# Kernel optimization log

Measured on AMD Instinct MI355X. Metric: run time of the kernel, lower is better.

## Reference

```python
import jax, jax.numpy as jnp
import numpy as np

VAR_SCALE = 0.1


def setup_inputs() -> dict:
    key = jax.random.key(0)
    k_x, k_tc, k_task, k_in, k_out = jax.random.split(key, 5)
    B, T, IN, OUT, R = 1024, 8, 4096, 4096, 64
    x = jax.random.normal(k_x, (B, T, IN), dtype=jnp.float32)
    tensor_core = jax.random.normal(k_tc, (R, R, R), dtype=jnp.float32) * VAR_SCALE
    task_core = jax.random.normal(k_task, (T, R), dtype=jnp.float32) * VAR_SCALE
    in_core = jax.random.normal(k_in, (IN, R), dtype=jnp.float32) * VAR_SCALE
    out_core = jax.random.normal(k_out, (OUT, R), dtype=jnp.float32) * VAR_SCALE
    return {"x": x, "tensor_core": tensor_core, "task_core": task_core,
            "in_core": in_core, "out_core": out_core}


def reference(x, tensor_core, task_core, in_core, out_core):
    # Tucker weight reconstruction, faithful to the torch einsum chain.
    # W1: [T, R, R] = task_core @ tensor_core (contract first core mode)
    W = jnp.einsum('tj,jkl->tkl', task_core, tensor_core)
    # W2: [T, IN, R] = contract in_core with middle mode
    W = jnp.einsum('ij,tjk->tik', in_core, W)
    # W3: [T, IN, OUT] = contract out_core with last mode
    W = jnp.einsum('oj,tij->tio', out_core, W)
    # Batched per-task matmul: x [B, T, IN] -> y [B, T, OUT]
    y = jnp.einsum('bti,tio->bto', x, W)
    return y
```

## Files before the change

kernel.cpp:

```cpp
#include <hip/hip_runtime.h>
#include <hip/hip_bf16.h>


typedef __bf16 bf16;
typedef __bf16 bf16x8 __attribute__((ext_vector_type(8)));
typedef __bf16 bf16x4 __attribute__((ext_vector_type(4)));
typedef float  f32x4  __attribute__((ext_vector_type(4)));

__device__ __forceinline__ bf16x8 load_frag_bf16(const bf16* p) {
    return *reinterpret_cast<const bf16x8*>(p);
}

__device__ __forceinline__ bf16x8 load_frag_f32(const float* p) {
    f32x4 a = *reinterpret_cast<const f32x4*>(p);
    f32x4 b = *reinterpret_cast<const f32x4*>(p + 4);
    bf16x8 r;
    r[0] = (bf16)a[0]; r[1] = (bf16)a[1]; r[2] = (bf16)a[2]; r[3] = (bf16)a[3];
    r[4] = (bf16)b[0]; r[5] = (bf16)b[1]; r[6] = (bf16)b[2]; r[7] = (bf16)b[3];
    return r;
}

__device__ __forceinline__ f32x4 mfma16(bf16x8 a, bf16x8 b, f32x4 c) {
    return __builtin_amdgcn_mfma_f32_16x16x32_bf16(a, b, c, 0, 0, 0);
}

__global__ __launch_bounds__(256) void k_setup(
    const float* __restrict__ task,
    const float* __restrict__ tensor,
    const float* __restrict__ in_core,
    bf16* __restrict__ w1,
    bf16* __restrict__ icT)
{
    int bid = blockIdx.x;
    if (bid < 128) {
        int t    = bid >> 4;
        int idx  = (bid & 15) * 256 + threadIdx.x;
        int j    = idx >> 6;
        int k    = idx & 63;
        float acc = 0.f;
        #pragma unroll 8
        for (int m = 0; m < 64; ++m)
            acc += task[t * 64 + m] * tensor[(m * 64 + j) * 64 + k];
        w1[(t * 64 + j) * 64 + k] = (bf16)acc;
    } else {
        int idx = (bid - 128) * 256 + threadIdx.x;
        int i0  = (idx & 511) * 8;
        int j   = idx >> 9;
        bf16x8 v;
        #pragma unroll
        for (int s = 0; s < 8; ++s)
            v[s] = (bf16)in_core[(size_t)(i0 + s) * 64 + j];
        *reinterpret_cast<bf16x8*>(icT + (size_t)j * 4096 + i0) = v;
    }
}

__global__ __launch_bounds__(256) void k2_mt(
    const float* __restrict__ out_core,
    const bf16* __restrict__ w1,
    bf16* __restrict__ mt)
{
    int t    = blockIdx.x >> 6;
    int ot   = blockIdx.x & 63;
    int wave = threadIdx.x >> 6;
    int lane = threadIdx.x & 63;
    int m    = lane & 15;
    int q    = lane >> 4;
    int o0   = ot * 64 + wave * 16;

    f32x4 acc[4] = {};
    #pragma unroll
    for (int kc = 0; kc < 64; kc += 32) {
        bf16x8 a = load_frag_f32(out_core + (size_t)(o0 + m) * 64 + kc + q * 8);
        #pragma unroll
        for (int nt = 0; nt < 4; ++nt) {
            bf16x8 b = load_frag_bf16(w1 + (size_t)(t * 64 + nt * 16 + m) * 64 + kc + q * 8);
            acc[nt] = mfma16(a, b, acc[nt]);
        }
    }
    #pragma unroll
    for (int nt = 0; nt < 4; ++nt) {
        #pragma unroll
        for (int r = 0; r < 4; ++r) {
            int o = o0 + q * 4 + r;
            mt[(size_t)(t * 4096 + o) * 64 + nt * 16 + m] = (bf16)acc[nt][r];
        }
    }
}

__global__ __launch_bounds__(256) void k_fused(
    const float* __restrict__ x,
    const bf16* __restrict__ icT,
    const bf16* __restrict__ mt,
    float* __restrict__ y)
{
    __shared__ bf16  xs[16 * 256];
    __shared__ bf16  zb[16 * 80];
    __shared__ float slab[4 * 2112];

    int t    = blockIdx.x & 7;
    int b0   = (blockIdx.x >> 3) * 16;
    int tid  = threadIdx.x;
    int r    = tid >> 4;
    int c16  = tid & 15;
    int wave = tid >> 6;
    int lane = tid & 63;
    int m    = lane & 15;
    int q    = lane >> 4;
    int n0   = wave * 16;

    const float* gsrc = x   + (size_t)((b0 + r) * 8 + t) * 4096;
    const bf16*  bbas = icT + (size_t)(n0 + m) * 4096;

    f32x4 vA[4], vB[4];
    #pragma unroll
    for (int i = 0; i < 4; ++i)
        vA[i] = *reinterpret_cast<const f32x4*>(gsrc + c16 * 4 + i * 64);
    #pragma unroll
    for (int i = 0; i < 4; ++i)
        vB[i] = *reinterpret_cast<const f32x4*>(gsrc + 256 + c16 * 4 + i * 64);

    f32x4 acc = {};
    #pragma unroll 1
    for (int kc = 0; kc < 4096; kc += 512) {
        __syncthreads();
        #pragma unroll
        for (int i = 0; i < 4; ++i) {
            bf16x4 w;
            w[0] = (bf16)vA[i][0]; w[1] = (bf16)vA[i][1];
            w[2] = (bf16)vA[i][2]; w[3] = (bf16)vA[i][3];
            int col = c16 * 4 + i * 64;
            int u   = (col >> 3) ^ (r & 7);
            *reinterpret_cast<bf16x4*>(&xs[r * 256 + u * 8 + (col & 7)]) = w;
        }
        __syncthreads();
        if (kc + 512 < 4096) {
            #pragma unroll
            for (int i = 0; i < 4; ++i)
                vA[i] = *reinterpret_cast<const f32x4*>(gsrc + kc + 512 + c16 * 4 + i * 64);
        }
        #pragma unroll
        for (int c = 0; c < 8; ++c) {
            int u = (c * 4 + q) ^ (m & 7);
            bf16x8 a = *reinterpret_cast<const bf16x8*>(&xs[m * 256 + u * 8]);
            bf16x8 b = load_frag_bf16(bbas + kc + c * 32 + q * 8);
            acc = mfma16(a, b, acc);
        }
        __syncthreads();
        #pragma unroll
        for (int i = 0; i < 4; ++i) {
            bf16x4 w;
            w[0] = (bf16)vB[i][0]; w[1] = (bf16)vB[i][1];
            w[2] = (bf16)vB[i][2]; w[3] = (bf16)vB[i][3];
            int col = c16 * 4 + i * 64;
            int u   = (col >> 3) ^ (r & 7);
            *reinterpret_cast<bf16x4*>(&xs[r * 256 + u * 8 + (col & 7)]) = w;
        }
        __syncthreads();
        if (kc + 768 < 4096) {
            #pragma unroll
            for (int i = 0; i < 4; ++i)
                vB[i] = *reinterpret_cast<const f32x4*>(gsrc + kc + 768 + c16 * 4 + i * 64);
        }
        #pragma unroll
        for (int c = 0; c < 8; ++c) {
            int u = (c * 4 + q) ^ (m & 7);
            bf16x8 a = *reinterpret_cast<const bf16x8*>(&xs[m * 256 + u * 8]);
            bf16x8 b = load_frag_bf16(bbas + kc + 256 + c * 32 + q * 8);
            acc = mfma16(a, b, acc);
        }
    }
    #pragma unroll
    for (int rr = 0; rr < 4; ++rr)
        zb[(q * 4 + rr) * 80 + n0 + m] = (bf16)acc[rr];
    __syncthreads();

    bf16x8 a_lo = *reinterpret_cast<const bf16x8*>(zb + m * 80 + q * 8);
    bf16x8 a_hi = *reinterpret_cast<const bf16x8*>(zb + m * 80 + 32 + q * 8);

    float* sw = slab + wave * 2112;
    const bf16* mbase = mt + ((size_t)t * 4096 + wave * 1024) * 64;

    #pragma unroll 1
    for (int g = 0; g < 8; ++g) {
        f32x4 acc2[8] = {};
        #pragma unroll
        for (int nt = 0; nt < 8; ++nt) {
            const bf16* bp = mbase + (size_t)(g * 128 + nt * 16 + m) * 64;
            bf16x8 blo = load_frag_bf16(bp + q * 8);
            bf16x8 bhi = load_frag_bf16(bp + 32 + q * 8);
            acc2[nt] = mfma16(a_lo, blo, acc2[nt]);
            acc2[nt] = mfma16(a_hi, bhi, acc2[nt]);
        }
        #pragma unroll
        for (int nt = 0; nt < 8; ++nt) {
            #pragma unroll
            for (int rr = 0; rr < 4; ++rr)
                sw[(q * 4 + rr) * 132 + nt * 16 + m] = acc2[nt][rr];
        }
        #pragma unroll
        for (int p = 0; p < 8; ++p) {
            int row = 2 * p + (lane >> 5);
            int cu  = lane & 31;
            f32x4 d = *reinterpret_cast<const f32x4*>(sw + row * 132 + cu * 4);
            *reinterpret_cast<f32x4*>(
                y + (size_t)((b0 + row) * 8 + t) * 4096 + wave * 1024 + g * 128 + cu * 4) = d;
        }
    }
}

extern "C" void kernel_launch(void* const* d_in, const int* in_sizes, int n_in,
                              void* d_out, int out_size, void* d_ws, size_t ws_size,
                              hipStream_t stream) {
    const float* x        = (const float*)d_in[0];
    const float* tensor_c = (const float*)d_in[1];
    const float* task_c   = (const float*)d_in[2];
    const float* in_c     = (const float*)d_in[3];
    const float* out_c    = (const float*)d_in[4];
    float* y = (float*)d_out;

    char* ws = (char*)d_ws;
    bf16* w1  = (bf16*)ws;
    bf16* icT = (bf16*)(ws + (64 << 10));
    bf16* mtc = (bf16*)(ws + (64 << 10) + (512 << 10));

    k_setup<<<256, 256, 0, stream>>>(task_c, tensor_c, in_c, w1, icT);
    k2_mt  <<<512, 256, 0, stream>>>(out_c, w1, mtc);
    k_fused<<<512, 256, 0, stream>>>(x, icT, mtc, y);
}
```

Baseline: 283.1 us.

## Halve batch tile, double-buffer x staging in LDS, double grid size

The fused kernel now processes 8 batch rows per block instead of 16, launching twice as many blocks. x chunks are staged into double-buffered LDS with one barrier per step, and B fragments are preloaded into registers, to overlap global loads with MFMA. The 16-row MFMA tiles duplicate the 8 rows, so half the compute is wasted. The out-core matrix is also re-read by twice as many blocks.

```diff
diff --git a/kernel.cpp b/kernel.cpp
--- a/kernel.cpp
+++ b/kernel.cpp
@@ -22,6 +22,12 @@
 
 __device__ __forceinline__ f32x4 mfma16(bf16x8 a, bf16x8 b, f32x4 c) {
     return __builtin_amdgcn_mfma_f32_16x16x32_bf16(a, b, c, 0, 0, 0);
+}
+
+__device__ __forceinline__ void bar_lgkm() {
+    asm volatile("s_waitcnt lgkmcnt(0)" ::: "memory");
+    __builtin_amdgcn_s_barrier();
+    __builtin_amdgcn_sched_barrier(0);
 }
 
 __global__ __launch_bounds__(256) void k_setup(
@@ -93,15 +99,15 @@
     const bf16* __restrict__ mt,
     float* __restrict__ y)
 {
-    __shared__ bf16  xs[16 * 256];
+    __shared__ bf16  xs[2][8 * 256];
     __shared__ bf16  zb[16 * 80];
-    __shared__ float slab[4 * 2112];
+    __shared__ float slab[4 * 1056];
 
     int t    = blockIdx.x & 7;
-    int b0   = (blockIdx.x >> 3) * 16;
+    int b0   = (blockIdx.x >> 3) * 8;
     int tid  = threadIdx.x;
-    int r    = tid >> 4;
-    int c16  = tid & 15;
+    int r    = tid >> 5;
+    int c32  = tid & 31;
     int wave = tid >> 6;
     int lane = tid & 63;
     int m    = lane & 15;
@@ -111,73 +117,80 @@
     const float* gsrc = x   + (size_t)((b0 + r) * 8 + t) * 4096;
     const bf16*  bbas = icT + (size_t)(n0 + m) * 4096;
 
-    f32x4 vA[4], vB[4];
-    #pragma unroll
-    for (int i = 0; i < 4; ++i)
-        vA[i] = *reinterpret_cast<const f32x4*>(gsrc + c16 * 4 + i * 64);
-    #pragma unroll
-    for (int i = 0; i < 4; ++i)
-        vB[i] = *reinterpret_cast<const f32x4*>(gsrc + 256 + c16 * 4 + i * 64);
-
+    auto stage = [&](bf16* buf, const f32x4* v) {
+        #pragma unroll
+        for (int i = 0; i < 2; ++i) {
+            bf16x4 w;
+            w[0] = (bf16)v[i][0]; w[1] = (bf16)v[i][1];
+            w[2] = (bf16)v[i][2]; w[3] = (bf16)v[i][3];
+            int col = c32 * 4 + i * 128;
+            int u   = (col >> 3) ^ r;
+            *reinterpret_cast<bf16x4*>(&buf[r * 256 + u * 8 + (col & 7)]) = w;
+        }
+    };
     f32x4 acc = {};
-    #pragma unroll 1
-    for (int kc = 0; kc < 4096; kc += 512) {
-        __syncthreads();
-        #pragma unroll
-        for (int i = 0; i < 4; ++i) {
-            bf16x4 w;
-            w[0] = (bf16)vA[i][0]; w[1] = (bf16)vA[i][1];
-            w[2] = (bf16)vA[i][2]; w[3] = (bf16)vA[i][3];
-            int col = c16 * 4 + i * 64;
-            int u   = (col >> 3) ^ (r & 7);
-            *reinterpret_cast<bf16x4*>(&xs[r * 256 + u * 8 + (col & 7)]) = w;
-        }
-        __syncthreads();
-        if (kc + 512 < 4096) {
-            #pragma unroll
-            for (int i = 0; i < 4; ++i)
-                vA[i] = *reinterpret_cast<const f32x4*>(gsrc + kc + 512 + c16 * 4 + i * 64);
-        }
+    auto compute = [&](const bf16* buf, const bf16x8* bfr) {
         #pragma unroll
         for (int c = 0; c < 8; ++c) {
             int u = (c * 4 + q) ^ (m & 7);
-            bf16x8 a = *reinterpret_cast<const bf16x8*>(&xs[m * 256 + u * 8]);
-            bf16x8 b = load_frag_bf16(bbas + kc + c * 32 + q * 8);
-            acc = mfma16(a, b, acc);
-        }
-        __syncthreads();
-        #pragma unroll
-        for (int i = 0; i < 4; ++i) {
-            bf16x4 w;
-            w[0] = (bf16)vB[i][0]; w[1] = (bf16)vB[i][1];
-            w[2] = (bf16)vB[i][2]; w[3] = (bf16)vB[i][3];
-            int col = c16 * 4 + i * 64;
-            int u   = (col >> 3) ^ (r & 7);
-            *reinterpret_cast<bf16x4*>(&xs[r * 256 + u * 8 + (col & 7)]) = w;
-        }
-        __syncthreads();
-        if (kc + 768 < 4096) {
+            bf16x8 a = *reinterpret_cast<const bf16x8*>(&buf[(m & 7) * 256 + u * 8]);
+            acc = mfma16(a, bfr[c], acc);
+        }
+    };
+
+    f32x4 vA[2], vB[2];
+    #pragma unroll
+    for (int i = 0; i < 2; ++i)
+        vA[i] = *reinterpret_cast<const f32x4*>(gsrc + c32 * 4 + i * 128);
+    #pragma unroll
+    for (int i = 0; i < 2; ++i)
+        vB[i] = *reinterpret_cast<const f32x4*>(gsrc + 256 + c32 * 4 + i * 128);
+
+    stage(xs[0], vA);
+    bar_lgkm();
+
+    #pragma unroll 1
+    for (int kt = 0; kt < 16; kt += 2) {
+        {
+            bf16x8 bfr[8];
             #pragma unroll
-            for (int i = 0; i < 4; ++i)
-                vB[i] = *reinterpret_cast<const f32x4*>(gsrc + kc + 768 + c16 * 4 + i * 64);
-        }
-        #pragma unroll
-        for (int c = 0; c < 8; ++c) {
-            int u = (c * 4 + q) ^ (m & 7);
-            bf16x8 a = *reinterpret_cast<const bf16x8*>(&xs[m * 256 + u * 8]);
-            bf16x8 b = load_frag_bf16(bbas + kc + 256 + c * 32 + q * 8);
-            acc = mfma16(a, b, acc);
+            for (int c = 0; c < 8; ++c)
+                bfr[c] = load_frag_bf16(bbas + kt * 256 + c * 32 + q * 8);
+            if (kt + 2 < 16) {
+                #pragma unroll
+                for (int i = 0; i < 2; ++i)
+                    vA[i] = *reinterpret_cast<const f32x4*>(
+                        gsrc + (kt + 2) * 256 + c32 * 4 + i * 128);
+            }
+            stage(xs[1], vB);
+            compute(xs[0], bfr);
+            bar_lgkm();
+        }
+        {
+            bf16x8 bfr[8];
+            #pragma unroll
+            for (int c = 0; c < 8; ++c)
+                bfr[c] = load_frag_bf16(bbas + (kt + 1) * 256 + c * 32 + q * 8);
+            if (kt + 3 < 16) {
+                #pragma unroll
+                for (int i = 0; i < 2; ++i)
+                    vB[i] = *reinterpret_cast<const f32x4*>(
+                        gsrc + (kt + 3) * 256 + c32 * 4 + i * 128);
+            }
+            if (kt + 2 < 16) stage(xs[0], vA);
+            compute(xs[1], bfr);
+            bar_lgkm();
         }
     }
     #pragma unroll
     for (int rr = 0; rr < 4; ++rr)
         zb[(q * 4 + rr) * 80 + n0 + m] = (bf16)acc[rr];
-    __syncthreads();
+    bar_lgkm();
 
     bf16x8 a_lo = *reinterpret_cast<const bf16x8*>(zb + m * 80 + q * 8);
     bf16x8 a_hi = *reinterpret_cast<const bf16x8*>(zb + m * 80 + 32 + q * 8);
 
-    float* sw = slab + wave * 2112;
+    float* sw = slab + wave * 1056;
     const bf16* mbase = mt + ((size_t)t * 4096 + wave * 1024) * 64;
 
     #pragma unroll 1
@@ -191,14 +204,16 @@
             acc2[nt] = mfma16(a_lo, blo, acc2[nt]);
             acc2[nt] = mfma16(a_hi, bhi, acc2[nt]);
         }
-        #pragma unroll
-        for (int nt = 0; nt < 8; ++nt) {
+        if (q < 2) {
             #pragma unroll
-            for (int rr = 0; rr < 4; ++rr)
-                sw[(q * 4 + rr) * 132 + nt * 16 + m] = acc2[nt][rr];
-        }
-        #pragma unroll
-        for (int p = 0; p < 8; ++p) {
+            for (int nt = 0; nt < 8; ++nt) {
+                #pragma unroll
+                for (int rr = 0; rr < 4; ++rr)
+                    sw[(q * 4 + rr) * 132 + nt * 16 + m] = acc2[nt][rr];
+            }
+        }
+        #pragma unroll
+        for (int p = 0; p < 4; ++p) {
             int row = 2 * p + (lane >> 5);
             int cu  = lane & 31;
             f32x4 d = *reinterpret_cast<const f32x4*>(sw + row * 132 + cu * 4);
@@ -223,7 +238,7 @@
     bf16* icT = (bf16*)(ws + (64 << 10));
     bf16* mtc = (bf16*)(ws + (64 << 10) + (512 << 10));
 
-    k_setup<<<256, 256, 0, stream>>>(task_c, tensor_c, in_c, w1, icT);
-    k2_mt  <<<512, 256, 0, stream>>>(out_c, w1, mtc);
-    k_fused<<<512, 256, 0, stream>>>(x, icT, mtc, y);
-}
+    k_setup<<<256,  256, 0, stream>>>(task_c, tensor_c, in_c, w1, icT);
+    k2_mt  <<<512,  256, 0, stream>>>(out_c, w1, mtc);
+    k_fused<<<1024, 256, 0, stream>>>(x, icT, mtc, y);
+}
```

After: 330.9 us. 1.17x slower.

## Stage x tiles with direct global-to-LDS loads and double-buffer B fragments

Applied to the files above, without the earlier changes.

The first GEMM stage of the fused kernel now loads fp32 x tiles straight into a double-buffered LDS pool with global_load_lds and an XOR swizzle. The bf16 conversion moves to the LDS read. The icT fragments are prefetched into registers one tile ahead, and a single waitcnt+barrier per tile replaces the earlier four syncthreads and register-staging round trips. The aim is more loads in flight and less VGPR pressure and barrier overhead. The cost is twice the LDS bytes for the fp32 tiles, a pool shared with the output slab, and conversion work on every LDS fragment read.

```diff
diff --git a/kernel.cpp b/kernel.cpp
--- a/kernel.cpp
+++ b/kernel.cpp
@@ -22,6 +22,16 @@
 
 __device__ __forceinline__ f32x4 mfma16(bf16x8 a, bf16x8 b, f32x4 c) {
     return __builtin_amdgcn_mfma_f32_16x16x32_bf16(a, b, c, 0, 0, 0);
+}
+
+__device__ __forceinline__ void gl_lds16(const float* g, void* l) {
+    __builtin_amdgcn_global_load_lds(
+        (const __attribute__((address_space(1))) void*)g,
+        (__attribute__((address_space(3))) void*)l, 16, 0, 0);
+}
+
+__device__ __forceinline__ void tile_bar() {
+    asm volatile("s_waitcnt vmcnt(0)\n\ts_barrier" ::: "memory");
 }
 
 __global__ __launch_bounds__(256) void k_setup(
@@ -93,81 +103,74 @@
     const bf16* __restrict__ mt,
     float* __restrict__ y)
 {
-    __shared__ bf16  xs[16 * 256];
-    __shared__ bf16  zb[16 * 80];
-    __shared__ float slab[4 * 2112];
+    __shared__ __align__(16) char pool[4 * 2112 * 4];
+    __shared__ bf16 zb[16 * 80];
+
+    float* xsf0 = (float*)pool;
+    float* xsf1 = (float*)pool + 4096;
+    float* slab = (float*)pool;
 
     int t    = blockIdx.x & 7;
     int b0   = (blockIdx.x >> 3) * 16;
     int tid  = threadIdx.x;
-    int r    = tid >> 4;
-    int c16  = tid & 15;
+    int row  = tid >> 4;
+    int cc   = (tid & 15) ^ row;
     int wave = tid >> 6;
     int lane = tid & 63;
     int m    = lane & 15;
     int q    = lane >> 4;
     int n0   = wave * 16;
 
-    const float* gsrc = x   + (size_t)((b0 + r) * 8 + t) * 4096;
+    const float* xrow = x + (size_t)((b0 + row) * 8 + t) * 4096 + cc * 4;
     const bf16*  bbas = icT + (size_t)(n0 + m) * 4096;
 
-    f32x4 vA[4], vB[4];
-    #pragma unroll
-    for (int i = 0; i < 4; ++i)
-        vA[i] = *reinterpret_cast<const f32x4*>(gsrc + c16 * 4 + i * 64);
-    #pragma unroll
-    for (int i = 0; i < 4; ++i)
-        vB[i] = *reinterpret_cast<const f32x4*>(gsrc + 256 + c16 * 4 + i * 64);
-
+    auto stage = [&](int kt, float* buf) {
+        char* lb = (char*)buf + wave * 1024;
+        const float* g = xrow + (size_t)kt * 256;
+        #pragma unroll
+        for (int i = 0; i < 4; ++i)
+            gl_lds16(g + i * 64, lb + i * 4096);
+    };
+    auto loadfrags = [&](bf16x8* f, int kt) {
+        #pragma unroll
+        for (int c = 0; c < 8; ++c)
+            f[c] = load_frag_bf16(bbas + kt * 256 + c * 32 + q * 8);
+    };
     f32x4 acc = {};
+    auto compute = [&](const float* buf, const bf16x8* f) {
+        #pragma unroll
+        for (int c = 0; c < 8; ++c) {
+            int ib = c >> 1;
+            int h2 = ((c & 1) * 4 + q) * 2;
+            const float* base = buf + ib * 1024 + m * 64;
+            f32x4 a0 = *reinterpret_cast<const f32x4*>(base + ((h2    ) ^ m) * 4);
+            f32x4 a1 = *reinterpret_cast<const f32x4*>(base + ((h2 + 1) ^ m) * 4);
+            bf16x8 a;
+            a[0] = (bf16)a0[0]; a[1] = (bf16)a0[1];
+            a[2] = (bf16)a0[2]; a[3] = (bf16)a0[3];
+            a[4] = (bf16)a1[0]; a[5] = (bf16)a1[1];
+            a[6] = (bf16)a1[2]; a[7] = (bf16)a1[3];
+            acc = mfma16(a, f[c], acc);
+        }
+    };
+
+    bf16x8 bfrA[8], bfrB[8];
+    loadfrags(bfrA, 0);
+    stage(0, xsf0);
+    tile_bar();
+
     #pragma unroll 1
-    for (int kc = 0; kc < 4096; kc += 512) {
-        __syncthreads();
-        #pragma unroll
-        for (int i = 0; i < 4; ++i) {
-            bf16x4 w;
-            w[0] = (bf16)vA[i][0]; w[1] = (bf16)vA[i][1];
-            w[2] = (bf16)vA[i][2]; w[3] = (bf16)vA[i][3];
-            int col = c16 * 4 + i * 64;
-            int u   = (col >> 3) ^ (r & 7);
-            *reinterpret_cast<bf16x4*>(&xs[r * 256 + u * 8 + (col & 7)]) = w;
-        }
-        __syncthreads();
-        if (kc + 512 < 4096) {
-            #pragma unroll
-            for (int i = 0; i < 4; ++i)
-                vA[i] = *reinterpret_cast<const f32x4*>(gsrc + kc + 512 + c16 * 4 + i * 64);
-        }
-        #pragma unroll
-        for (int c = 0; c < 8; ++c) {
-            int u = (c * 4 + q) ^ (m & 7);
-            bf16x8 a = *reinterpret_cast<const bf16x8*>(&xs[m * 256 + u * 8]);
-            bf16x8 b = load_frag_bf16(bbas + kc + c * 32 + q * 8);
-            acc = mfma16(a, b, acc);
-        }
-        __syncthreads();
-        #pragma unroll
-        for (int i = 0; i < 4; ++i) {
-            bf16x4 w;
-            w[0] = (bf16)vB[i][0]; w[1] = (bf16)vB[i][1];
-            w[2] = (bf16)vB[i][2]; w[3] = (bf16)vB[i][3];
-            int col = c16 * 4 + i * 64;
-            int u   = (col >> 3) ^ (r & 7);
-            *reinterpret_cast<bf16x4*>(&xs[r * 256 + u * 8 + (col & 7)]) = w;
-        }
-        __syncthreads();
-        if (kc + 768 < 4096) {
-            #pragma unroll
-            for (int i = 0; i < 4; ++i)
-                vB[i] = *reinterpret_cast<const f32x4*>(gsrc + kc + 768 + c16 * 4 + i * 64);
-        }
-        #pragma unroll
-        for (int c = 0; c < 8; ++c) {
-            int u = (c * 4 + q) ^ (m & 7);
-            bf16x8 a = *reinterpret_cast<const bf16x8*>(&xs[m * 256 + u * 8]);
-            bf16x8 b = load_frag_bf16(bbas + kc + 256 + c * 32 + q * 8);
-            acc = mfma16(a, b, acc);
-        }
+    for (int kt = 0; kt < 16; kt += 2) {
+        stage(kt + 1, xsf1);
+        loadfrags(bfrB, kt + 1);
+        compute(xsf0, bfrA);
+        tile_bar();
+        if (kt + 2 < 16) {
+            stage(kt + 2, xsf0);
+            loadfrags(bfrA, kt + 2);
+        }
+        compute(xsf1, bfrB);
+        tile_bar();
     }
     #pragma unroll
     for (int rr = 0; rr < 4; ++rr)
@@ -199,11 +202,11 @@
         }
         #pragma unroll
         for (int p = 0; p < 8; ++p) {
-            int row = 2 * p + (lane >> 5);
-            int cu  = lane & 31;
-            f32x4 d = *reinterpret_cast<const f32x4*>(sw + row * 132 + cu * 4);
+            int rr = 2 * p + (lane >> 5);
+            int cu = lane & 31;
+            f32x4 d = *reinterpret_cast<const f32x4*>(sw + rr * 132 + cu * 4);
             *reinterpret_cast<f32x4*>(
-                y + (size_t)((b0 + row) * 8 + t) * 4096 + wave * 1024 + g * 128 + cu * 4) = d;
+                y + (size_t)((b0 + rr) * 8 + t) * 4096 + wave * 1024 + g * 128 + cu * 4) = d;
         }
     }
 }
```

Result: no change. 284.8 us (+0.6%).
